# Performance work log

Measured on AMD Instinct MI355X. Metric: run time of the kernel, lower is better.

## Reference

```python
import jax, jax.numpy as jnp
import numpy as np

H = 16
D_MODEL = 1024
D_K = D_MODEL // H
NWORDS = 16384


def setup_inputs() -> dict:
    key0 = jax.random.key(0)
    ks = jax.random.split(key0, 11)
    s = 0.02
    return {
        "query": jax.random.normal(ks[0], (1, D_MODEL), dtype=jnp.float32),
        "key": jax.random.normal(ks[1], (NWORDS, D_MODEL), dtype=jnp.float32),
        "value": jax.random.normal(ks[2], (NWORDS, D_MODEL), dtype=jnp.float32),
        "Wq": jax.random.normal(ks[3], (D_MODEL, D_MODEL), dtype=jnp.float32) * s,
        "bq": jax.random.normal(ks[4], (D_MODEL,), dtype=jnp.float32) * s,
        "Wk": jax.random.normal(ks[5], (D_MODEL, D_MODEL), dtype=jnp.float32) * s,
        "bk": jax.random.normal(ks[6], (D_MODEL,), dtype=jnp.float32) * s,
        "Wv": jax.random.normal(ks[7], (D_MODEL, D_MODEL), dtype=jnp.float32) * s,
        "bv": jax.random.normal(ks[8], (D_MODEL,), dtype=jnp.float32) * s,
        "Wo": jax.random.normal(ks[9], (D_MODEL, D_MODEL), dtype=jnp.float32) * s,
        "bo": jax.random.normal(ks[10], (D_MODEL,), dtype=jnp.float32) * s,
    }


def reference(query, key, value, Wq, bq, Wk, bk, Wv, bv, Wo, bo):
    # torch Linear: y = x @ W.T + b
    q = (query @ Wq.T + bq).reshape(H, D_K)          # [h, d_k]  (single query token)
    k = (key @ Wk.T + bk).reshape(-1, H, D_K)        # [n, h, d_k]
    v = (value @ Wv.T + bv).reshape(-1, H, D_K)      # [n, h, d_k]
    # NOTE: original module applies NO 1/sqrt(d_k) scaling.
    scores = jnp.einsum("hd,nhd->hn", q, k)          # [h, n]
    p_attn = jax.nn.softmax(scores, axis=-1)          # dropout p=0 -> no-op
    x = jnp.einsum("hn,nhd->hd", p_attn, v).reshape(1, H * D_K)  # [1, d_model]
    return x @ Wo.T + bo                              # [1, d_model]
```

## Files before the change

### kernel.cpp

```cpp
#include <hip/hip_runtime.h>

#define DM 1024
#define NW 16384

typedef __attribute__((ext_vector_type(8))) short short8;
typedef __attribute__((ext_vector_type(4))) float f32x4;

#define OFF_AH   1024
#define OFF_AL   9216
#define OFF_D0   17408
#define OFF_SP   17440
#define OFF_X    25632
#define OFF_W    26656
#define OFF_PART 49152

__device__ __forceinline__ unsigned short f2bf(float f) {
  unsigned int u = __float_as_uint(f);
  return (unsigned short)((u + 0x7fffu + ((u >> 16) & 1u)) >> 16);
}

__global__ __launch_bounds__(256) void k_rowdot(const float* __restrict__ W,
                                                const float* __restrict__ v,
                                                const float* __restrict__ b,
                                                float* __restrict__ out) {
  const int wave = (blockIdx.x * 256 + threadIdx.x) >> 6;
  const int lane = threadIdx.x & 63;
  const float* row = W + (size_t)wave * DM + 4 * lane;
  float s = 0.f;
#pragma unroll
  for (int j = 0; j < 4; ++j) {
    float4 a = *(const float4*)(row + j * 256);
    float4 x = *(const float4*)(v + j * 256 + 4 * lane);
    s += a.x * x.x + a.y * x.y + a.z * x.z + a.w * x.w;
  }
#pragma unroll
  for (int off = 32; off; off >>= 1) s += __shfl_xor(s, off, 64);
  if (lane == 0) out[wave] = s + b[wave];
}

__global__ __launch_bounds__(256) void k_qck(const float* __restrict__ Wq,
                                             const float* __restrict__ bq,
                                             const float* __restrict__ query,
                                             const float* __restrict__ Wk,
                                             const float* __restrict__ bk,
                                             short* __restrict__ Ah,
                                             short* __restrict__ Al,
                                             float* __restrict__ d0,
                                             float* __restrict__ w) {
  const int h = blockIdx.x >> 2;
  const int mc = blockIdx.x & 3;
  const int t = threadIdx.x;
  const int lane = t & 63;
  const int wv = t >> 6;
  __shared__ float qh[64];
  w[blockIdx.x * 256 + t] = 0.f;
  float4 qv[4];
#pragma unroll
  for (int j = 0; j < 4; ++j) qv[j] = *(const float4*)(query + j * 256 + 4 * lane);
#pragma unroll 1
  for (int ii = 0; ii < 16; ii += 4) {
    float4 a[4][4];
#pragma unroll
    for (int r = 0; r < 4; ++r) {
      const float* rp = Wq + (size_t)(h * 64 + 4 * (ii + r) + wv) * DM + 4 * lane;
#pragma unroll
      for (int j = 0; j < 4; ++j) a[r][j] = *(const float4*)(rp + j * 256);
    }
    float s[4] = {0.f, 0.f, 0.f, 0.f};
#pragma unroll
    for (int r = 0; r < 4; ++r)
#pragma unroll
      for (int j = 0; j < 4; ++j)
        s[r] += a[r][j].x * qv[j].x + a[r][j].y * qv[j].y +
                a[r][j].z * qv[j].z + a[r][j].w * qv[j].w;
#pragma unroll
    for (int off = 32; off; off >>= 1)
#pragma unroll
      for (int r = 0; r < 4; ++r) s[r] += __shfl_xor(s[r], off, 64);
    if (lane == 0)
#pragma unroll
      for (int r = 0; r < 4; ++r)
        qh[4 * (ii + r) + wv] = s[r] + bq[h * 64 + 4 * (ii + r) + wv];
  }
  __syncthreads();
  const int m = mc * 256 + t;
  const float* Wp = Wk + (size_t)(h * 64) * DM + m;
  float s = 0.f;
#pragma unroll 2
  for (int db = 0; db < 8; ++db) {
    float wv8[8];
#pragma unroll
    for (int j = 0; j < 8; ++j) wv8[j] = Wp[(size_t)(db * 8 + j) * DM];
#pragma unroll
    for (int j = 0; j < 8; ++j) s = fmaf(qh[db * 8 + j], wv8[j], s);
  }
  unsigned short hu = f2bf(s);
  float hf = __uint_as_float(((unsigned int)hu) << 16);
  unsigned short lu = f2bf(s - hf);
  const int kb = m >> 5, q = (m >> 3) & 3, j = m & 7;
  const int idx = (kb * 64 + q * 16 + h) * 8 + j;
  Ah[idx] = (short)hu;
  Al[idx] = (short)lu;
  if (mc == 0 && t == 0) {
    float tt = 0.f;
    for (int d = 0; d < 64; ++d) tt += qh[d] * bk[h * 64 + d];
    d0[h] = tt;
  }
}

__global__ __launch_bounds__(256, 2) void k_spv(const float* __restrict__ key,
                                                const float* __restrict__ value,
                                                const short* __restrict__ AhG,
                                                const short* __restrict__ AlG,
                                                const float* __restrict__ d0,
                                                float* __restrict__ part,
                                                float* __restrict__ Spart) {
  const int nb = blockIdx.x;
  const int t = threadIdx.x;
  const int lane = t & 63;
  const int wv = t >> 6;
  const int tile = wv >> 1;
  const int khalf = wv & 1;
  const int nl = tile * 16 + (lane & 15);
  const int n = nb * 32 + nl;
  const int quad = lane >> 4;
  const float* base = key + (size_t)n * DM + quad * 8;
  const short8* A8h = (const short8*)AhG;
  const short8* A8l = (const short8*)AlG;
  __shared__ float el[32 * 16];
  __shared__ f32x4 sred[4][64];

  short8 ah[2][4], al[2][4];
  float4 f0[2][4], f1[2][4];
  f32x4 acc0 = {0.f, 0.f, 0.f, 0.f};
  f32x4 acc1 = {0.f, 0.f, 0.f, 0.f};

#define LOADG(buf, g) { \
  _Pragma("unroll") for (int i = 0; i < 4; ++i) { \
    const int kb = khalf * 16 + (g) * 4 + i; \
    ah[buf][i] = A8h[kb * 64 + lane]; \
    al[buf][i] = A8l[kb * 64 + lane]; \
    f0[buf][i] = *(const float4*)(base + kb * 32); \
    f1[buf][i] = *(const float4*)(base + kb * 32 + 4); \
  } }

#define PROC(buf) { \
  _Pragma("unroll") for (int i = 0; i < 4; ++i) { \
    float ff[8] = {f0[buf][i].x, f0[buf][i].y, f0[buf][i].z, f0[buf][i].w, \
                   f1[buf][i].x, f1[buf][i].y, f1[buf][i].z, f1[buf][i].w}; \
    short8 bh, bl; \
    _Pragma("unroll") for (int j = 0; j < 8; ++j) { \
      unsigned short hu = f2bf(ff[j]); \
      bh[j] = (short)hu; \
      float hf = __uint_as_float(((unsigned int)hu) << 16); \
      bl[j] = (short)f2bf(ff[j] - hf); \
    } \
    if ((i & 1) == 0) { \
      acc0 = __builtin_amdgcn_mfma_f32_16x16x32_bf16(ah[buf][i], bh, acc0, 0, 0, 0); \
      acc0 = __builtin_amdgcn_mfma_f32_16x16x32_bf16(ah[buf][i], bl, acc0, 0, 0, 0); \
      acc0 = __builtin_amdgcn_mfma_f32_16x16x32_bf16(al[buf][i], bh, acc0, 0, 0, 0); \
    } else { \
      acc1 = __builtin_amdgcn_mfma_f32_16x16x32_bf16(ah[buf][i], bh, acc1, 0, 0, 0); \
      acc1 = __builtin_amdgcn_mfma_f32_16x16x32_bf16(ah[buf][i], bl, acc1, 0, 0, 0); \
      acc1 = __builtin_amdgcn_mfma_f32_16x16x32_bf16(al[buf][i], bh, acc1, 0, 0, 0); \
    } \
  } }

  LOADG(0, 0)
  LOADG(1, 1)
  PROC(0) LOADG(0, 2)
  PROC(1) LOADG(1, 3)
  PROC(0)
  PROC(1)
#undef LOADG
#undef PROC

  f32x4 at = acc0 + acc1;
  sred[wv][lane] = at;
  __syncthreads();
  if (khalf == 0) {
    f32x4 o = sred[wv + 1][lane];
    const float4 dv = *(const float4*)(d0 + quad * 4);
    float ex0 = __expf(at[0] + o[0] + dv.x);
    float ex1 = __expf(at[1] + o[1] + dv.y);
    float ex2 = __expf(at[2] + o[2] + dv.z);
    float ex3 = __expf(at[3] + o[3] + dv.w);
    *(float4*)&el[nl * 16 + quad * 4] = make_float4(ex0, ex1, ex2, ex3);
  }
  __syncthreads();
  if (t < 16) {
    float s = 0.f;
#pragma unroll
    for (int r = 0; r < 32; ++r) s += el[r * 16 + t];
    Spart[t * 512 + nb] = s;
  }

  float4 acc[16];
#pragma unroll
  for (int h = 0; h < 16; ++h) acc[h] = make_float4(0.f, 0.f, 0.f, 0.f);
  const float* vp = value + (size_t)(nb * 32) * DM + 4 * t;
  float4 vbuf[2][8];

#define LOADV(buf, g) { \
  _Pragma("unroll") for (int i = 0; i < 8; ++i) \
    vbuf[buf][i] = *(const float4*)(vp + (size_t)((g) * 8 + i) * DM); }

#define COMPV(buf, g) { \
  _Pragma("unroll") for (int i = 0; i < 8; ++i) { \
    const float4* er4 = (const float4*)&el[((g) * 8 + i) * 16]; \
    float4 e0 = er4[0], e1 = er4[1], e2 = er4[2], e3 = er4[3]; \
    float4 vvv = vbuf[buf][i]; \
    acc[0].x  = fmaf(e0.x, vvv.x, acc[0].x);  acc[0].y  = fmaf(e0.x, vvv.y, acc[0].y); \
    acc[0].z  = fmaf(e0.x, vvv.z, acc[0].z);  acc[0].w  = fmaf(e0.x, vvv.w, acc[0].w); \
    acc[1].x  = fmaf(e0.y, vvv.x, acc[1].x);  acc[1].y  = fmaf(e0.y, vvv.y, acc[1].y); \
    acc[1].z  = fmaf(e0.y, vvv.z, acc[1].z);  acc[1].w  = fmaf(e0.y, vvv.w, acc[1].w); \
    acc[2].x  = fmaf(e0.z, vvv.x, acc[2].x);  acc[2].y  = fmaf(e0.z, vvv.y, acc[2].y); \
    acc[2].z  = fmaf(e0.z, vvv.z, acc[2].z);  acc[2].w  = fmaf(e0.z, vvv.w, acc[2].w); \
    acc[3].x  = fmaf(e0.w, vvv.x, acc[3].x);  acc[3].y  = fmaf(e0.w, vvv.y, acc[3].y); \
    acc[3].z  = fmaf(e0.w, vvv.z, acc[3].z);  acc[3].w  = fmaf(e0.w, vvv.w, acc[3].w); \
    acc[4].x  = fmaf(e1.x, vvv.x, acc[4].x);  acc[4].y  = fmaf(e1.x, vvv.y, acc[4].y); \
    acc[4].z  = fmaf(e1.x, vvv.z, acc[4].z);  acc[4].w  = fmaf(e1.x, vvv.w, acc[4].w); \
    acc[5].x  = fmaf(e1.y, vvv.x, acc[5].x);  acc[5].y  = fmaf(e1.y, vvv.y, acc[5].y); \
    acc[5].z  = fmaf(e1.y, vvv.z, acc[5].z);  acc[5].w  = fmaf(e1.y, vvv.w, acc[5].w); \
    acc[6].x  = fmaf(e1.z, vvv.x, acc[6].x);  acc[6].y  = fmaf(e1.z, vvv.y, acc[6].y); \
    acc[6].z  = fmaf(e1.z, vvv.z, acc[6].z);  acc[6].w  = fmaf(e1.z, vvv.w, acc[6].w); \
    acc[7].x  = fmaf(e1.w, vvv.x, acc[7].x);  acc[7].y  = fmaf(e1.w, vvv.y, acc[7].y); \
    acc[7].z  = fmaf(e1.w, vvv.z, acc[7].z);  acc[7].w  = fmaf(e1.w, vvv.w, acc[7].w); \
    acc[8].x  = fmaf(e2.x, vvv.x, acc[8].x);  acc[8].y  = fmaf(e2.x, vvv.y, acc[8].y); \
    acc[8].z  = fmaf(e2.x, vvv.z, acc[8].z);  acc[8].w  = fmaf(e2.x, vvv.w, acc[8].w); \
    acc[9].x  = fmaf(e2.y, vvv.x, acc[9].x);  acc[9].y  = fmaf(e2.y, vvv.y, acc[9].y); \
    acc[9].z  = fmaf(e2.y, vvv.z, acc[9].z);  acc[9].w  = fmaf(e2.y, vvv.w, acc[9].w); \
    acc[10].x = fmaf(e2.z, vvv.x, acc[10].x); acc[10].y = fmaf(e2.z, vvv.y, acc[10].y); \
    acc[10].z = fmaf(e2.z, vvv.z, acc[10].z); acc[10].w = fmaf(e2.z, vvv.w, acc[10].w); \
    acc[11].x = fmaf(e2.w, vvv.x, acc[11].x); acc[11].y = fmaf(e2.w, vvv.y, acc[11].y); \
    acc[11].z = fmaf(e2.w, vvv.z, acc[11].z); acc[11].w = fmaf(e2.w, vvv.w, acc[11].w); \
    acc[12].x = fmaf(e3.x, vvv.x, acc[12].x); acc[12].y = fmaf(e3.x, vvv.y, acc[12].y); \
    acc[12].z = fmaf(e3.x, vvv.z, acc[12].z); acc[12].w = fmaf(e3.x, vvv.w, acc[12].w); \
    acc[13].x = fmaf(e3.y, vvv.x, acc[13].x); acc[13].y = fmaf(e3.y, vvv.y, acc[13].y); \
    acc[13].z = fmaf(e3.y, vvv.z, acc[13].z); acc[13].w = fmaf(e3.y, vvv.w, acc[13].w); \
    acc[14].x = fmaf(e3.z, vvv.x, acc[14].x); acc[14].y = fmaf(e3.z, vvv.y, acc[14].y); \
    acc[14].z = fmaf(e3.z, vvv.z, acc[14].z); acc[14].w = fmaf(e3.z, vvv.w, acc[14].w); \
    acc[15].x = fmaf(e3.w, vvv.x, acc[15].x); acc[15].y = fmaf(e3.w, vvv.y, acc[15].y); \
    acc[15].z = fmaf(e3.w, vvv.z, acc[15].z); acc[15].w = fmaf(e3.w, vvv.w, acc[15].w); \
  } }

  LOADV(0, 0)
  LOADV(1, 1)
  COMPV(0, 0) LOADV(0, 2)
  COMPV(1, 1) LOADV(1, 3)
  COMPV(0, 2)
  COMPV(1, 3)
#undef LOADV
#undef COMPV

  float* pp = part + (size_t)nb * (16 * DM) + 4 * t;
#pragma unroll
  for (int h = 0; h < 16; ++h) *(float4*)(pp + (size_t)h * DM) = acc[h];
}

__global__ __launch_bounds__(256) void k_wred(const float* __restrict__ part,
                                              float* __restrict__ w) {
  const int g = blockIdx.x * 256 + threadIdx.x;
  const int o = g & 16383;
  const int q = g >> 14;
  float s = 0.f;
#pragma unroll 1
  for (int ib = 0; ib < 16; ++ib) {
    float x[8];
#pragma unroll
    for (int j = 0; j < 8; ++j)
      x[j] = part[(size_t)(q * 128 + ib * 8 + j) * 16384 + o];
#pragma unroll
    for (int j = 0; j < 8; ++j) s += x[j];
  }
  atomicAdd(w + o, s);
}

__global__ __launch_bounds__(256) void k_xproj(const float* __restrict__ Wv,
                                               const float* __restrict__ w,
                                               const float* __restrict__ bv,
                                               const float* __restrict__ Spart,
                                               float* __restrict__ x) {
  const int wave = (blockIdx.x * 256 + threadIdx.x) >> 6;
  const int lane = threadIdx.x & 63;
  const int h = wave >> 6;
  const float* vec = w + (size_t)h * DM;
  const float* row = Wv + (size_t)wave * DM + 4 * lane;
  const float* sp = Spart + (size_t)h * 512;
  float s = 0.f, ss = 0.f;
#pragma unroll
  for (int i = 0; i < 8; ++i) ss += sp[i * 64 + lane];
#pragma unroll
  for (int j = 0; j < 4; ++j) {
    float4 a = *(const float4*)(row + j * 256);
    float4 x4 = *(const float4*)(vec + j * 256 + 4 * lane);
    s += a.x * x4.x + a.y * x4.y + a.z * x4.z + a.w * x4.w;
  }
#pragma unroll
  for (int off = 32; off; off >>= 1) {
    s += __shfl_xor(s, off, 64);
    ss += __shfl_xor(ss, off, 64);
  }
  if (lane == 0) x[wave] = s / ss + bv[wave];
}

extern "C" void kernel_launch(void* const* d_in, const int* in_sizes, int n_in,
                              void* d_out, int out_size, void* d_ws, size_t ws_size,
                              hipStream_t stream) {
  const float* query = (const float*)d_in[0];
  const float* key   = (const float*)d_in[1];
  const float* value = (const float*)d_in[2];
  const float* Wq    = (const float*)d_in[3];
  const float* bq    = (const float*)d_in[4];
  const float* Wk    = (const float*)d_in[5];
  const float* bk    = (const float*)d_in[6];
  const float* Wv    = (const float*)d_in[7];
  const float* bv    = (const float*)d_in[8];
  const float* Wo    = (const float*)d_in[9];
  const float* bo    = (const float*)d_in[10];
  float* out = (float*)d_out;
  float* ws  = (float*)d_ws;
  short* Ah  = (short*)(ws + OFF_AH);
  short* Al  = (short*)(ws + OFF_AL);

  k_qck    <<<64,  256, 0, stream>>>(Wq, bq, query, Wk, bk, Ah, Al,
                                     ws + OFF_D0, ws + OFF_W);
  k_spv    <<<512, 256, 0, stream>>>(key, value, Ah, Al, ws + OFF_D0,
                                     ws + OFF_PART, ws + OFF_SP);
  k_wred   <<<256, 256, 0, stream>>>(ws + OFF_PART, ws + OFF_W);
  k_xproj  <<<256, 256, 0, stream>>>(Wv, ws + OFF_W, bv, ws + OFF_SP, ws + OFF_X);
  k_rowdot <<<256, 256, 0, stream>>>(Wo, ws + OFF_X, bo, out);
}
```

Measured before the change: 208.8 us.

## Double k_spv block to 512 threads, splitting K into quarters and halving V columns

The score/PV kernel now runs 8 waves per block instead of 4. Each tile's key dot product is split across four K-quarters instead of two, and the partial sums are reduced through shared memory before the exp. In the P·V phase each thread handles 2 value columns instead of 4, which halves accumulator registers and allows higher occupancy. This adds more latency hiding and parallelism for the memory-bound key/value streaming, at the cost of more shared-memory reduction traffic and narrower float2 loads and stores.

```diff
diff --git a/kernel.cpp b/kernel.cpp
--- a/kernel.cpp
+++ b/kernel.cpp
@@ -108,7 +108,7 @@
   }
 }
 
-__global__ __launch_bounds__(256, 2) void k_spv(const float* __restrict__ key,
+__global__ __launch_bounds__(512, 4) void k_spv(const float* __restrict__ key,
                                                 const float* __restrict__ value,
                                                 const short* __restrict__ AhG,
                                                 const short* __restrict__ AlG,
@@ -119,16 +119,17 @@
   const int t = threadIdx.x;
   const int lane = t & 63;
   const int wv = t >> 6;
-  const int tile = wv >> 1;
-  const int khalf = wv & 1;
-  const int nl = tile * 16 + (lane & 15);
+  const int tile = wv >> 2;
+  const int kq = wv & 3;
+  const int row16 = lane & 15;
+  const int nl = tile * 16 + row16;
   const int n = nb * 32 + nl;
   const int quad = lane >> 4;
   const float* base = key + (size_t)n * DM + quad * 8;
   const short8* A8h = (const short8*)AhG;
   const short8* A8l = (const short8*)AlG;
   __shared__ float el[32 * 16];
-  __shared__ f32x4 sred[4][64];
+  __shared__ f32x4 sred[8][64];
 
   short8 ah[2][4], al[2][4];
   float4 f0[2][4], f1[2][4];
@@ -137,7 +138,7 @@
 
 #define LOADG(buf, g) { \
   _Pragma("unroll") for (int i = 0; i < 4; ++i) { \
-    const int kb = khalf * 16 + (g) * 4 + i; \
+    const int kb = kq * 8 + (g) * 4 + i; \
     ah[buf][i] = A8h[kb * 64 + lane]; \
     al[buf][i] = A8l[kb * 64 + lane]; \
     f0[buf][i] = *(const float4*)(base + kb * 32); \
@@ -168,8 +169,6 @@
 
   LOADG(0, 0)
   LOADG(1, 1)
-  PROC(0) LOADG(0, 2)
-  PROC(1) LOADG(1, 3)
   PROC(0)
   PROC(1)
 #undef LOADG
@@ -178,16 +177,19 @@
   f32x4 at = acc0 + acc1;
   sred[wv][lane] = at;
   __syncthreads();
-  if (khalf == 0) {
-    f32x4 o = sred[wv + 1][lane];
+  if (kq == 0) {
+    f32x4 o1 = sred[wv + 1][lane];
+    f32x4 o2 = sred[wv + 2][lane];
+    f32x4 o3 = sred[wv + 3][lane];
     const float4 dv = *(const float4*)(d0 + quad * 4);
-    float ex0 = __expf(at[0] + o[0] + dv.x);
-    float ex1 = __expf(at[1] + o[1] + dv.y);
-    float ex2 = __expf(at[2] + o[2] + dv.z);
-    float ex3 = __expf(at[3] + o[3] + dv.w);
+    float ex0 = __expf(at[0] + o1[0] + o2[0] + o3[0] + dv.x);
+    float ex1 = __expf(at[1] + o1[1] + o2[1] + o3[1] + dv.y);
+    float ex2 = __expf(at[2] + o1[2] + o2[2] + o3[2] + dv.z);
+    float ex3 = __expf(at[3] + o1[3] + o2[3] + o3[3] + dv.w);
     *(float4*)&el[nl * 16 + quad * 4] = make_float4(ex0, ex1, ex2, ex3);
   }
   __syncthreads();
+
   if (t < 16) {
     float s = 0.f;
 #pragma unroll
@@ -195,67 +197,49 @@
     Spart[t * 512 + nb] = s;
   }
 
-  float4 acc[16];
-#pragma unroll
-  for (int h = 0; h < 16; ++h) acc[h] = make_float4(0.f, 0.f, 0.f, 0.f);
-  const float* vp = value + (size_t)(nb * 32) * DM + 4 * t;
-  float4 vbuf[2][8];
-
-#define LOADV(buf, g) { \
-  _Pragma("unroll") for (int i = 0; i < 8; ++i) \
-    vbuf[buf][i] = *(const float4*)(vp + (size_t)((g) * 8 + i) * DM); }
-
-#define COMPV(buf, g) { \
+  float2 acc[16];
+#pragma unroll
+  for (int h = 0; h < 16; ++h) acc[h] = make_float2(0.f, 0.f);
+  const float* vp = value + (size_t)(nb * 32) * DM + 2 * t;
+  float2 vbA[8], vbB[8];
+
+#define LOADV(VB, G) { _Pragma("unroll") for (int i = 0; i < 8; ++i) \
+    VB[i] = *(const float2*)(vp + (size_t)((G) * 8 + i) * DM); }
+#define COMPV(VB, G) { \
   _Pragma("unroll") for (int i = 0; i < 8; ++i) { \
-    const float4* er4 = (const float4*)&el[((g) * 8 + i) * 16]; \
+    const float4* er4 = (const float4*)&el[((G) * 8 + i) * 16]; \
     float4 e0 = er4[0], e1 = er4[1], e2 = er4[2], e3 = er4[3]; \
-    float4 vvv = vbuf[buf][i]; \
+    float2 vvv = VB[i]; \
     acc[0].x  = fmaf(e0.x, vvv.x, acc[0].x);  acc[0].y  = fmaf(e0.x, vvv.y, acc[0].y); \
-    acc[0].z  = fmaf(e0.x, vvv.z, acc[0].z);  acc[0].w  = fmaf(e0.x, vvv.w, acc[0].w); \
     acc[1].x  = fmaf(e0.y, vvv.x, acc[1].x);  acc[1].y  = fmaf(e0.y, vvv.y, acc[1].y); \
-    acc[1].z  = fmaf(e0.y, vvv.z, acc[1].z);  acc[1].w  = fmaf(e0.y, vvv.w, acc[1].w); \
     acc[2].x  = fmaf(e0.z, vvv.x, acc[2].x);  acc[2].y  = fmaf(e0.z, vvv.y, acc[2].y); \
-    acc[2].z  = fmaf(e0.z, vvv.z, acc[2].z);  acc[2].w  = fmaf(e0.z, vvv.w, acc[2].w); \
     acc[3].x  = fmaf(e0.w, vvv.x, acc[3].x);  acc[3].y  = fmaf(e0.w, vvv.y, acc[3].y); \
-    acc[3].z  = fmaf(e0.w, vvv.z, acc[3].z);  acc[3].w  = fmaf(e0.w, vvv.w, acc[3].w); \
     acc[4].x  = fmaf(e1.x, vvv.x, acc[4].x);  acc[4].y  = fmaf(e1.x, vvv.y, acc[4].y); \
-    acc[4].z  = fmaf(e1.x, vvv.z, acc[4].z);  acc[4].w  = fmaf(e1.x, vvv.w, acc[4].w); \
     acc[5].x  = fmaf(e1.y, vvv.x, acc[5].x);  acc[5].y  = fmaf(e1.y, vvv.y, acc[5].y); \
-    acc[5].z  = fmaf(e1.y, vvv.z, acc[5].z);  acc[5].w  = fmaf(e1.y, vvv.w, acc[5].w); \
     acc[6].x  = fmaf(e1.z, vvv.x, acc[6].x);  acc[6].y  = fmaf(e1.z, vvv.y, acc[6].y); \
-    acc[6].z  = fmaf(e1.z, vvv.z, acc[6].z);  acc[6].w  = fmaf(e1.z, vvv.w, acc[6].w); \
     acc[7].x  = fmaf(e1.w, vvv.x, acc[7].x);  acc[7].y  = fmaf(e1.w, vvv.y, acc[7].y); \
-    acc[7].z  = fmaf(e1.w, vvv.z, acc[7].z);  acc[7].w  = fmaf(e1.w, vvv.w, acc[7].w); \
     acc[8].x  = fmaf(e2.x, vvv.x, acc[8].x);  acc[8].y  = fmaf(e2.x, vvv.y, acc[8].y); \
-    acc[8].z  = fmaf(e2.x, vvv.z, acc[8].z);  acc[8].w  = fmaf(e2.x, vvv.w, acc[8].w); \
     acc[9].x  = fmaf(e2.y, vvv.x, acc[9].x);  acc[9].y  = fmaf(e2.y, vvv.y, acc[9].y); \
-    acc[9].z  = fmaf(e2.y, vvv.z, acc[9].z);  acc[9].w  = fmaf(e2.y, vvv.w, acc[9].w); \
     acc[10].x = fmaf(e2.z, vvv.x, acc[10].x); acc[10].y = fmaf(e2.z, vvv.y, acc[10].y); \
-    acc[10].z = fmaf(e2.z, vvv.z, acc[10].z); acc[10].w = fmaf(e2.z, vvv.w, acc[10].w); \
     acc[11].x = fmaf(e2.w, vvv.x, acc[11].x); acc[11].y = fmaf(e2.w, vvv.y, acc[11].y); \
-    acc[11].z = fmaf(e2.w, vvv.z, acc[11].z); acc[11].w = fmaf(e2.w, vvv.w, acc[11].w); \
     acc[12].x = fmaf(e3.x, vvv.x, acc[12].x); acc[12].y = fmaf(e3.x, vvv.y, acc[12].y); \
-    acc[12].z = fmaf(e3.x, vvv.z, acc[12].z); acc[12].w = fmaf(e3.x, vvv.w, acc[12].w); \
     acc[13].x = fmaf(e3.y, vvv.x, acc[13].x); acc[13].y = fmaf(e3.y, vvv.y, acc[13].y); \
-    acc[13].z = fmaf(e3.y, vvv.z, acc[13].z); acc[13].w = fmaf(e3.y, vvv.w, acc[13].w); \
     acc[14].x = fmaf(e3.z, vvv.x, acc[14].x); acc[14].y = fmaf(e3.z, vvv.y, acc[14].y); \
-    acc[14].z = fmaf(e3.z, vvv.z, acc[14].z); acc[14].w = fmaf(e3.z, vvv.w, acc[14].w); \
     acc[15].x = fmaf(e3.w, vvv.x, acc[15].x); acc[15].y = fmaf(e3.w, vvv.y, acc[15].y); \
-    acc[15].z = fmaf(e3.w, vvv.z, acc[15].z); acc[15].w = fmaf(e3.w, vvv.w, acc[15].w); \
   } }
 
-  LOADV(0, 0)
-  LOADV(1, 1)
-  COMPV(0, 0) LOADV(0, 2)
-  COMPV(1, 1) LOADV(1, 3)
-  COMPV(0, 2)
-  COMPV(1, 3)
+  LOADV(vbA, 0)
+  LOADV(vbB, 1)
+  COMPV(vbA, 0) LOADV(vbA, 2)
+  COMPV(vbB, 1) LOADV(vbB, 3)
+  COMPV(vbA, 2)
+  COMPV(vbB, 3)
 #undef LOADV
 #undef COMPV
 
-  float* pp = part + (size_t)nb * (16 * DM) + 4 * t;
-#pragma unroll
-  for (int h = 0; h < 16; ++h) *(float4*)(pp + (size_t)h * DM) = acc[h];
+  float* pp = part + (size_t)nb * (16 * DM) + 2 * t;
+#pragma unroll
+  for (int h = 0; h < 16; ++h) *(float2*)(pp + (size_t)h * DM) = acc[h];
 }
 
 __global__ __launch_bounds__(256) void k_wred(const float* __restrict__ part,
@@ -325,7 +309,7 @@
 
   k_qck    <<<64,  256, 0, stream>>>(Wq, bq, query, Wk, bk, Ah, Al,
                                      ws + OFF_D0, ws + OFF_W);
-  k_spv    <<<512, 256, 0, stream>>>(key, value, Ah, Al, ws + OFF_D0,
+  k_spv    <<<512, 512, 0, stream>>>(key, value, Ah, Al, ws + OFF_D0,
                                      ws + OFF_PART, ws + OFF_SP);
   k_wred   <<<256, 256, 0, stream>>>(ws + OFF_PART, ws + OFF_W);
   k_xproj  <<<256, 256, 0, stream>>>(Wv, ws + OFF_W, bv, ws + OFF_SP, ws + OFF_X);
```

After: 209.6 us. Within noise of the previous version (+0.4%).
